# Performance work log

Hardware: AMD Instinct MI355X
Metric: run time of the kernel (lower is better)

Reference implementation:

```python
import jax, jax.numpy as jnp
import numpy as np
from jax import lax

B, N, S, H = 8, 32, 512, 768   # batch, max spans, seq len, bert hidden
K, C, L = 3, 128, 64           # conv kernel height, cnn_hidden_size, num labels


def setup_inputs() -> dict:
    key = jax.random.key(0)
    ks = jax.random.split(key, 9)
    rng = np.random.default_rng(0)
    W = 16  # max span width
    starts = rng.integers(0, S - W, size=(B, N))
    widths = rng.integers(1, W + 1, size=(B, N))
    starts[0, 0], widths[0, 0] = 100, W        # force max span width = 16
    starts[0, 1], widths[0, 1] = S - W, 1      # force max prefix width = 496
    starts[0, 2], widths[0, 2] = 0, 1          # force min end = 1 -> max suffix = 511
    ends = starts + widths
    spans_dranges = jnp.asarray(np.stack([starts, ends], axis=-1), dtype=jnp.int32)
    sc = 0.02
    return {
        "tokens_emb": jax.random.normal(ks[0], (B, S, H), jnp.float32),
        "span_w": jax.random.normal(ks[1], (C, H, K), jnp.float32) * sc,
        "span_b": jax.random.normal(ks[2], (C,), jnp.float32) * sc,
        "prefix_w": jax.random.normal(ks[3], (C, H, K), jnp.float32) * sc,
        "prefix_b": jax.random.normal(ks[4], (C,), jnp.float32) * sc,
        "suffix_w": jax.random.normal(ks[5], (C, H, K), jnp.float32) * sc,
        "suffix_b": jax.random.normal(ks[6], (C,), jnp.float32) * sc,
        "fc_w": jax.random.normal(ks[7], (L, 3 * C), jnp.float32) * sc,
        "fc_b": jax.random.normal(ks[8], (L,), jnp.float32) * sc,
        "spans_dranges": spans_dranges,
        "word_seq_lengths": jnp.full((B,), S, dtype=jnp.int32),
        "max_span_width": W,
        "max_prefix_width": S - W,
        "max_suffix_width": S - 1,
    }


def _conv_pool(x, w, b):
    # x: [BN, T, H]; Conv2d(H->C, kernel (K,1)) over time + max_pool over all valid positions
    T = x.shape[1]
    if T < K:  # original pads with zeros up to kernel size
        x = jnp.pad(x, ((0, 0), (0, K - T), (0, 0)))
    y = lax.conv_general_dilated(x.transpose(0, 2, 1), w, (1,), 'VALID',
                                 dimension_numbers=('NCH', 'OIH', 'NCH'))  # [BN, C, T-K+1]
    return (y + b[None, :, None]).max(axis=2)  # pool_filter_size == full output length


def reference(tokens_emb, span_w, span_b, prefix_w, prefix_b, suffix_w, suffix_b,
              fc_w, fc_b, spans_dranges, word_seq_lengths,
              max_span_width, max_prefix_width, max_suffix_width):
    starts = spans_dranges[..., 0]  # [B,N]
    ends = spans_dranges[..., 1]

    def gather(idx, mask):
        # idx, mask: [B,N,W] -> zero-padded per-span token embeddings [B*N, W, H]
        g = jnp.take_along_axis(tokens_emb[:, None], jnp.clip(idx, 0, S - 1)[..., None], axis=2)
        return (g * mask[..., None]).reshape(B * N, -1, H)

    ar = jnp.arange(max_span_width)
    span_x = gather(starts[..., None] + ar, ar < (ends - starts)[..., None])
    arp = jnp.arange(max_prefix_width)
    prefix_x = gather(jnp.broadcast_to(arp, (B, N, max_prefix_width)), arp < starts[..., None])
    ars = jnp.arange(max_suffix_width)
    suffix_x = gather(ends[..., None] + ars,
                      ars < (word_seq_lengths[:, None, None] - ends[..., None]))

    feats = jnp.concatenate([
        _conv_pool(prefix_x, prefix_w, prefix_b),
        _conv_pool(span_x, span_w, span_b),
        _conv_pool(suffix_x, suffix_w, suffix_b),
    ], axis=-1)  # [B*N, 3C]
    probs = jax.nn.sigmoid(feats @ fc_w.T + fc_b)  # [B*N, L]
    pred_ids = (probs > 0.5).astype(jnp.int32).reshape(B, N, L)
    return probs, pred_ids
```

## Files before the change

kernel.cpp:

```cpp
#include <hip/hip_runtime.h>
#include <hip/hip_bf16.h>
#include <math.h>

#define NEG_INF (-1e30f)

typedef _Float16 half8 __attribute__((ext_vector_type(8)));
typedef _Float16 half4 __attribute__((ext_vector_type(4)));
typedef _Float16 half2v __attribute__((ext_vector_type(2)));
typedef float f32x4 __attribute__((ext_vector_type(4)));

__device__ __forceinline__ void load_lds16(const void* g, void* l) {
  __builtin_amdgcn_global_load_lds((const __attribute__((address_space(1))) void*)g,
                                   (__attribute__((address_space(3))) void*)l, 16, 0, 0);
}

__global__ __launch_bounds__(256) void prep(
    const float* __restrict__ tokens, const float* __restrict__ span_w,
    const float* __restrict__ prefix_w, const float* __restrict__ suffix_w,
    const float* __restrict__ fc_w, _Float16* __restrict__ A2,
    _Float16* __restrict__ Bt, float* __restrict__ fcT) {
  int bid = blockIdx.x;
  int t = threadIdx.x;
  if (bid < 3072) {
    int g4 = (bid * 256 + t) * 4;
    int m = g4 / 768, h = g4 % 768;
    float4 x = *(const float4*)(tokens + g4);
    float xs[4] = {x.x, x.y, x.z, x.w};
    half4 hi, lo, hi6;
#pragma unroll
    for (int i = 0; i < 4; ++i) {
      _Float16 h_ = (_Float16)xs[i];
      hi[i] = h_;
      lo[i] = (_Float16)((xs[i] - (float)h_) * 64.0f);
      hi6[i] = (_Float16)((float)h_ * 0.015625f);
    }
    size_t base = (size_t)m * 2304 + h;
    *(half4*)(A2 + base) = hi;
    *(half4*)(A2 + base + 768) = lo;
    *(half4*)(A2 + base + 1536) = hi6;
  } else if (bid < 3648) {
    int idx = (bid - 3072) * 256 + t;
    int ws = idx / 49152;
    int r = idx % 49152;
    int c = r / 384, h = (r % 384) * 2;
    const float* wsrc = (ws == 0) ? prefix_w : (ws == 1) ? span_w : suffix_w;
    const float* wp = wsrc + (size_t)(c * 768 + h) * 3;
#pragma unroll
    for (int tap = 0; tap < 3; ++tap) {
      float w0 = wp[tap], w1 = wp[3 + tap];
      _Float16 h0 = (_Float16)w0, h1 = (_Float16)w1;
      half2v r0 = {h0, h1};
      half2v r1 = {(_Float16)((float)h0 * 0.015625f),
                   (_Float16)((float)h1 * 0.015625f)};
      half2v r2 = {(_Float16)((w0 - (float)h0) * 64.0f),
                   (_Float16)((w1 - (float)h1) * 64.0f)};
      size_t jb = (size_t)(ws * 384 + tap * 128 + c) * 2304 + h;
      *(half2v*)(Bt + jb) = r0;
      *(half2v*)(Bt + jb + 768) = r1;
      *(half2v*)(Bt + jb + 1536) = r2;
    }
  } else {
    int g = (bid - 3648) * 256 + t;
    int i = g >> 6, c = g & 63;
    fcT[g] = fc_w[c * 384 + i];
  }
}

__global__ __launch_bounds__(256) void gemm_f16(const _Float16* __restrict__ A2,
                                                const _Float16* __restrict__ Bt,
                                                float* __restrict__ Ct) {
  __shared__ _Float16 As[2][64 * 32];
  __shared__ _Float16 Bs[2][128 * 32];
  const int bm = blockIdx.x * 64;
  const int bj = blockIdx.y * 128;
  const int tid = threadIdx.x;
  const int w = tid >> 6;
  const int lane = tid & 63;
  const int row = tid >> 2;
  const int koff = (tid & 3) * 8;
  const _Float16* gA = A2 + (size_t)(bm + row) * 2304 + koff;
  const _Float16* gB0 = Bt + (size_t)(bj + row) * 2304 + koff;
  const _Float16* gB1 = Bt + (size_t)(bj + 64 + row) * 2304 + koff;
  const int mrow = lane & 15;
  const int kq = (lane >> 4) * 8;
  const int m0w = (w & 1) * 32;
  const int n0w = (w >> 1) * 64;
  f32x4 acc[2][4];
#pragma unroll
  for (int i = 0; i < 2; ++i)
#pragma unroll
    for (int j = 0; j < 4; ++j) acc[i][j] = (f32x4){0.f, 0.f, 0.f, 0.f};

  load_lds16(gA, &As[0][w * 512]);
  load_lds16(gB0, &Bs[0][w * 512]);
  load_lds16(gB1, &Bs[0][2048 + w * 512]);

  int cur = 0;
  for (int k0 = 0; k0 < 2304; k0 += 32) {
    __syncthreads();
    if (k0 + 32 < 2304) {
      int nxt = cur ^ 1;
      load_lds16(gA + k0 + 32, &As[nxt][w * 512]);
      load_lds16(gB0 + k0 + 32, &Bs[nxt][w * 512]);
      load_lds16(gB1 + k0 + 32, &Bs[nxt][2048 + w * 512]);
    }
    half8 a0 = *(const half8*)&As[cur][(m0w + mrow) * 32 + kq];
    half8 a1 = *(const half8*)&As[cur][(m0w + 16 + mrow) * 32 + kq];
#pragma unroll
    for (int nt = 0; nt < 4; ++nt) {
      half8 b = *(const half8*)&Bs[cur][(n0w + nt * 16 + mrow) * 32 + kq];
      acc[0][nt] = __builtin_amdgcn_mfma_f32_16x16x32_f16(a0, b, acc[0][nt], 0, 0, 0);
      acc[1][nt] = __builtin_amdgcn_mfma_f32_16x16x32_f16(a1, b, acc[1][nt], 0, 0, 0);
    }
    cur ^= 1;
  }
  const int mbase = bm + m0w + (lane >> 4) * 4;
#pragma unroll
  for (int mt = 0; mt < 2; ++mt)
#pragma unroll
    for (int nt = 0; nt < 4; ++nt) {
      int n_out = bj + n0w + nt * 16 + mrow;
      *(f32x4*)(Ct + (size_t)n_out * 4096 + mbase + mt * 16) = acc[mt][nt];
    }
}

__global__ __launch_bounds__(256) void scan_kernel(const float* __restrict__ Ct,
                                                   const int* __restrict__ wsl,
                                                   float* __restrict__ PM2,
                                                   float* __restrict__ SM2) {
  int pair = blockIdx.x * 4 + (threadIdx.x >> 6);
  int b = pair >> 7;
  int c = pair & 127;
  int lane = threadIdx.x & 63;
  int mb = b * 512;
  int t0 = lane * 8;
  const float* p0 = Ct + (size_t)(0 + c) * 4096 + mb;
  const float* p1 = Ct + (size_t)(128 + c) * 4096 + mb;
  const float* p2 = Ct + (size_t)(256 + c) * 4096 + mb;
  float v[8];
#pragma unroll
  for (int i = 0; i < 8; i++) {
    int t = t0 + i;
    v[i] = (t < 494) ? (p0[t] + p1[t + 1] + p2[t + 2]) : NEG_INF;
  }
#pragma unroll
  for (int i = 1; i < 8; i++) v[i] = fmaxf(v[i], v[i - 1]);
  float x = v[7];
#pragma unroll
  for (int d = 1; d < 64; d <<= 1) {
    float y = __shfl_up(x, d);
    if (lane >= d) x = fmaxf(x, y);
  }
  float excl = __shfl_up(x, 1);
  if (lane == 0) excl = NEG_INF;
  float* pm = PM2 + (size_t)pair * 512;
#pragma unroll
  for (int i = 0; i < 8; i++) {
    int t = t0 + i;
    if (t < 494) pm[t] = fmaxf(v[i], excl);
  }
  const float* s0 = Ct + (size_t)(768 + c) * 4096 + mb;
  const float* s1 = Ct + (size_t)(896 + c) * 4096 + mb;
  const float* s2 = Ct + (size_t)(1024 + c) * 4096 + mb;
  int qmax = wsl[b] - 3;
  if (qmax > 509) qmax = 509;
  float u[8];
#pragma unroll
  for (int i = 0; i < 8; i++) {
    int q = t0 + i;
    u[i] = (q <= qmax) ? (s0[q] + s1[q + 1] + s2[q + 2]) : NEG_INF;
  }
#pragma unroll
  for (int i = 6; i >= 0; i--) u[i] = fmaxf(u[i], u[i + 1]);
  float xr = u[0];
#pragma unroll
  for (int d = 1; d < 64; d <<= 1) {
    float y = __shfl_down(xr, d);
    if (lane < 64 - d) xr = fmaxf(xr, y);
  }
  float exclr = __shfl_down(xr, 1);
  if (lane == 63) exclr = NEG_INF;
  float* sm = SM2 + (size_t)pair * 512;
#pragma unroll
  for (int i = 0; i < 8; i++) sm[t0 + i] = fmaxf(u[i], exclr);
}

__global__ __launch_bounds__(128) void span_kernel(
    const float* __restrict__ Ct, const float* __restrict__ PM2,
    const float* __restrict__ SM2, const float* __restrict__ prefix_b,
    const float* __restrict__ span_b, const float* __restrict__ suffix_b,
    const float* __restrict__ fcT, const float* __restrict__ fc_b,
    const int* __restrict__ spans, const int* __restrict__ wsl,
    float* __restrict__ out) {
  __shared__ float sfeat[384];
  __shared__ float part[64];
  int sp = blockIdx.x;
  int b = sp >> 5;
  int c = threadIdx.x;
  int s = spans[sp * 2], e = spans[sp * 2 + 1];
  int Lb = wsl[b];
  int mb = b * 512;
  {
    const float* t0p = Ct + (size_t)c * 4096 + mb;
    const float* t1p = Ct + (size_t)(128 + c) * 4096 + mb;
    float m = NEG_INF;
    if (s >= 3) m = fmaxf(m, PM2[(size_t)(b * 128 + c) * 512 + s - 3]);
    if (s >= 2 && s <= 495) m = fmaxf(m, t0p[s - 2] + t1p[s - 1]);
    if (s >= 1 && s <= 494) m = fmaxf(m, t0p[s - 1]);
    if (s <= 493) m = fmaxf(m, 0.0f);
    sfeat[c] = m + prefix_b[c];
  }
  {
    const float* u0 = Ct + (size_t)(384 + c) * 4096 + mb;
    const float* u1 = Ct + (size_t)(512 + c) * 4096 + mb;
    const float* u2 = Ct + (size_t)(640 + c) * 4096 + mb;
    int w = e - s;
    float m = NEG_INF;
    for (int p = 0; p + 2 < w; ++p)
      m = fmaxf(m, u0[s + p] + u1[s + p + 1] + u2[s + p + 2]);
    if (w >= 2 && w <= 15) m = fmaxf(m, u0[s + w - 2] + u1[s + w - 1]);
    if (w <= 14) m = fmaxf(m, u0[s + w - 1]);
    if (w <= 13) m = fmaxf(m, 0.0f);
    sfeat[128 + c] = m + span_b[c];
  }
  {
    const float* x0 = Ct + (size_t)(768 + c) * 4096 + mb;
    const float* x1 = Ct + (size_t)(896 + c) * 4096 + mb;
    float m = NEG_INF;
    if (e <= Lb - 3) m = fmaxf(m, SM2[(size_t)(b * 128 + c) * 512 + e]);
    if (Lb - 2 - e >= 0 && Lb - 2 - e <= 508)
      m = fmaxf(m, x0[Lb - 2] + x1[Lb - 1]);
    if (Lb - 1 - e >= 0 && Lb - 1 - e <= 508) m = fmaxf(m, x0[Lb - 1]);
    if (Lb - e <= 508) m = fmaxf(m, 0.0f);
    sfeat[256 + c] = m + suffix_b[c];
  }
  __syncthreads();
  {
    int cc = threadIdx.x & 63;
    int half = threadIdx.x >> 6;
    float acc2 = 0.0f;
    const float* fp = fcT + (size_t)(half * 192) * 64 + cc;
    const float* sf = sfeat + half * 192;
#pragma unroll 8
    for (int i = 0; i < 192; ++i) acc2 = fmaf(sf[i], fp[(size_t)i * 64], acc2);
    if (half) part[cc] = acc2;
    __syncthreads();
    if (!half) {
      float a = acc2 + part[cc] + fc_b[cc];
      float pr = 1.0f / (1.0f + expf(-a));
      out[sp * 64 + cc] = pr;
      out[16384 + sp * 64 + cc] = (pr > 0.5f) ? 1.0f : 0.0f;
    }
  }
}

extern "C" void kernel_launch(void* const* d_in, const int* in_sizes, int n_in,
                              void* d_out, int out_size, void* d_ws,
                              size_t ws_size, hipStream_t stream) {
  const float* tokens = (const float*)d_in[0];
  const float* span_w = (const float*)d_in[1];
  const float* span_b = (const float*)d_in[2];
  const float* prefix_w = (const float*)d_in[3];
  const float* prefix_b = (const float*)d_in[4];
  const float* suffix_w = (const float*)d_in[5];
  const float* suffix_b = (const float*)d_in[6];
  const float* fc_w = (const float*)d_in[7];
  const float* fc_b = (const float*)d_in[8];
  const int* spans = (const int*)d_in[9];
  const int* wsl = (const int*)d_in[10];
  float* out = (float*)d_out;

  char* ws = (char*)d_ws;
  float* Ct = (float*)ws;
  _Float16* A2 = (_Float16*)(ws + 18874368);
  _Float16* Bt = (_Float16*)(ws + 37748736);
  float* PM2 = (float*)(ws + 43057152);
  float* SM2 = (float*)(ws + 45154304);
  float* fcT = (float*)(ws + 47251456);

  hipLaunchKernelGGL(prep, dim3(3744), dim3(256), 0, stream, tokens, span_w,
                     prefix_w, suffix_w, fc_w, A2, Bt, fcT);
  hipLaunchKernelGGL(gemm_f16, dim3(64, 9), dim3(256), 0, stream, A2, Bt, Ct);
  hipLaunchKernelGGL(scan_kernel, dim3(256), dim3(256), 0, stream, Ct, wsl,
                     PM2, SM2);
  hipLaunchKernelGGL(span_kernel, dim3(256), dim3(128), 0, stream, Ct, PM2,
                     SM2, prefix_b, span_b, suffix_b, fcT, fc_b, spans, wsl,
                     out);
}
```

Measured before the change: 156.2 us.

## Double GEMM K-tile to 64 with XOR-swizzled LDS layout and vectorize weight prep

The GEMM now stages 64-wide K tiles in LDS instead of 32, so the loop takes half as many iterations and barriers and issues more MFMAs per sync. LDS columns are XOR-swizzled by row to avoid bank conflicts on the half8 fragment reads. The weight-prep path now has each thread convert 8 values with float4 loads and half8 stores instead of 2 scalar values, using fewer blocks. This doubles LDS use per block, which may lower occupancy.

```diff
diff --git a/kernel.cpp b/kernel.cpp
--- a/kernel.cpp
+++ b/kernel.cpp
@@ -6,7 +6,6 @@
 
 typedef _Float16 half8 __attribute__((ext_vector_type(8)));
 typedef _Float16 half4 __attribute__((ext_vector_type(4)));
-typedef _Float16 half2v __attribute__((ext_vector_type(2)));
 typedef float f32x4 __attribute__((ext_vector_type(4)));
 
 __device__ __forceinline__ void load_lds16(const void* g, void* l) {
@@ -38,29 +37,34 @@
     *(half4*)(A2 + base) = hi;
     *(half4*)(A2 + base + 768) = lo;
     *(half4*)(A2 + base + 1536) = hi6;
-  } else if (bid < 3648) {
-    int idx = (bid - 3072) * 256 + t;
-    int ws = idx / 49152;
-    int r = idx % 49152;
-    int c = r / 384, h = (r % 384) * 2;
+  } else if (bid < 3216) {
+    int g = (bid - 3072) * 256 + t;
+    int ws = g / 12288;
+    int r = g % 12288;
+    int c = r / 96, h = (r % 96) * 8;
     const float* wsrc = (ws == 0) ? prefix_w : (ws == 1) ? span_w : suffix_w;
-    const float* wp = wsrc + (size_t)(c * 768 + h) * 3;
+    const float* src = wsrc + (size_t)(c * 768 + h) * 3;
+    float wv[24];
+#pragma unroll
+    for (int i = 0; i < 6; ++i) *(float4*)&wv[i * 4] = *(const float4*)(src + i * 4);
 #pragma unroll
     for (int tap = 0; tap < 3; ++tap) {
-      float w0 = wp[tap], w1 = wp[3 + tap];
-      _Float16 h0 = (_Float16)w0, h1 = (_Float16)w1;
-      half2v r0 = {h0, h1};
-      half2v r1 = {(_Float16)((float)h0 * 0.015625f),
-                   (_Float16)((float)h1 * 0.015625f)};
-      half2v r2 = {(_Float16)((w0 - (float)h0) * 64.0f),
-                   (_Float16)((w1 - (float)h1) * 64.0f)};
+      half8 hi, lo, hi6;
+#pragma unroll
+      for (int i = 0; i < 8; ++i) {
+        float x = wv[i * 3 + tap];
+        _Float16 h_ = (_Float16)x;
+        hi[i] = h_;
+        lo[i] = (_Float16)((x - (float)h_) * 64.0f);
+        hi6[i] = (_Float16)((float)h_ * 0.015625f);
+      }
       size_t jb = (size_t)(ws * 384 + tap * 128 + c) * 2304 + h;
-      *(half2v*)(Bt + jb) = r0;
-      *(half2v*)(Bt + jb + 768) = r1;
-      *(half2v*)(Bt + jb + 1536) = r2;
+      *(half8*)(Bt + jb) = hi;
+      *(half8*)(Bt + jb + 768) = hi6;
+      *(half8*)(Bt + jb + 1536) = lo;
     }
   } else {
-    int g = (bid - 3648) * 256 + t;
+    int g = (bid - 3216) * 256 + t;
     int i = g >> 6, c = g & 63;
     fcT[g] = fc_w[c * 384 + i];
   }
@@ -69,22 +73,24 @@
 __global__ __launch_bounds__(256) void gemm_f16(const _Float16* __restrict__ A2,
                                                 const _Float16* __restrict__ Bt,
                                                 float* __restrict__ Ct) {
-  __shared__ _Float16 As[2][64 * 32];
-  __shared__ _Float16 Bs[2][128 * 32];
+  __shared__ _Float16 As[2][64 * 64];
+  __shared__ _Float16 Bs[2][128 * 64];
   const int bm = blockIdx.x * 64;
   const int bj = blockIdx.y * 128;
   const int tid = threadIdx.x;
   const int w = tid >> 6;
   const int lane = tid & 63;
-  const int row = tid >> 2;
-  const int koff = (tid & 3) * 8;
-  const _Float16* gA = A2 + (size_t)(bm + row) * 2304 + koff;
-  const _Float16* gB0 = Bt + (size_t)(bj + row) * 2304 + koff;
-  const _Float16* gB1 = Bt + (size_t)(bj + 64 + row) * 2304 + koff;
+  const int lr = lane >> 3;
+  const int kcs = (lane & 7) ^ lr;
+  const _Float16* gA = A2 + (size_t)(bm + w * 8 + lr) * 2304 + kcs * 8;
+  const _Float16* gB = Bt + (size_t)(bj + w * 8 + lr) * 2304 + kcs * 8;
   const int mrow = lane & 15;
-  const int kq = (lane >> 4) * 8;
+  const int qb = lane >> 4;
+  const int sw = lane & 7;
   const int m0w = (w & 1) * 32;
   const int n0w = (w >> 1) * 64;
+  const int co0 = (qb ^ sw) * 8;
+  const int co1 = ((qb + 4) ^ sw) * 8;
   f32x4 acc[2][4];
 #pragma unroll
   for (int i = 0; i < 2; ++i)
@@ -92,25 +98,34 @@
     for (int j = 0; j < 4; ++j) acc[i][j] = (f32x4){0.f, 0.f, 0.f, 0.f};
 
   load_lds16(gA, &As[0][w * 512]);
-  load_lds16(gB0, &Bs[0][w * 512]);
-  load_lds16(gB1, &Bs[0][2048 + w * 512]);
+  load_lds16(gA + 32 * 2304, &As[0][2048 + w * 512]);
+#pragma unroll
+  for (int p = 0; p < 4; ++p)
+    load_lds16(gB + (size_t)p * 32 * 2304, &Bs[0][p * 2048 + w * 512]);
 
   int cur = 0;
-  for (int k0 = 0; k0 < 2304; k0 += 32) {
+  for (int k0 = 0; k0 < 2304; k0 += 64) {
     __syncthreads();
-    if (k0 + 32 < 2304) {
+    if (k0 + 64 < 2304) {
       int nxt = cur ^ 1;
-      load_lds16(gA + k0 + 32, &As[nxt][w * 512]);
-      load_lds16(gB0 + k0 + 32, &Bs[nxt][w * 512]);
-      load_lds16(gB1 + k0 + 32, &Bs[nxt][2048 + w * 512]);
-    }
-    half8 a0 = *(const half8*)&As[cur][(m0w + mrow) * 32 + kq];
-    half8 a1 = *(const half8*)&As[cur][(m0w + 16 + mrow) * 32 + kq];
-#pragma unroll
-    for (int nt = 0; nt < 4; ++nt) {
-      half8 b = *(const half8*)&Bs[cur][(n0w + nt * 16 + mrow) * 32 + kq];
-      acc[0][nt] = __builtin_amdgcn_mfma_f32_16x16x32_f16(a0, b, acc[0][nt], 0, 0, 0);
-      acc[1][nt] = __builtin_amdgcn_mfma_f32_16x16x32_f16(a1, b, acc[1][nt], 0, 0, 0);
+      load_lds16(gA + k0 + 64, &As[nxt][w * 512]);
+      load_lds16(gA + k0 + 64 + 32 * 2304, &As[nxt][2048 + w * 512]);
+#pragma unroll
+      for (int p = 0; p < 4; ++p)
+        load_lds16(gB + k0 + 64 + (size_t)p * 32 * 2304,
+                   &Bs[nxt][p * 2048 + w * 512]);
+    }
+#pragma unroll
+    for (int ks = 0; ks < 2; ++ks) {
+      const int co = ks ? co1 : co0;
+      half8 a0 = *(const half8*)&As[cur][(m0w + mrow) * 64 + co];
+      half8 a1 = *(const half8*)&As[cur][(m0w + 16 + mrow) * 64 + co];
+#pragma unroll
+      for (int nt = 0; nt < 4; ++nt) {
+        half8 b = *(const half8*)&Bs[cur][(n0w + nt * 16 + mrow) * 64 + co];
+        acc[0][nt] = __builtin_amdgcn_mfma_f32_16x16x32_f16(a0, b, acc[0][nt], 0, 0, 0);
+        acc[1][nt] = __builtin_amdgcn_mfma_f32_16x16x32_f16(a1, b, acc[1][nt], 0, 0, 0);
+      }
     }
     cur ^= 1;
   }
@@ -278,7 +293,7 @@
   float* SM2 = (float*)(ws + 45154304);
   float* fcT = (float*)(ws + 47251456);
 
-  hipLaunchKernelGGL(prep, dim3(3744), dim3(256), 0, stream, tokens, span_w,
+  hipLaunchKernelGGL(prep, dim3(3312), dim3(256), 0, stream, tokens, span_w,
                      prefix_w, suffix_w, fc_w, A2, Bt, fcT);
   hipLaunchKernelGGL(gemm_f16, dim3(64, 9), dim3(256), 0, stream, A2, Bt, Ct);
   hipLaunchKernelGGL(scan_kernel, dim3(256), dim3(256), 0, stream, Ct, wsl,
```

Result: no change. 153.3 us (-1.8%).
